# Performance work log

Measured on AMD Instinct MI355X. Metric: run time of the kernel, lower is better.

The kernel has to match this reference:

```python
import jax, jax.numpy as jnp
import numpy as np


def setup_inputs() -> dict:
    key = jax.random.key(0)
    k1, k2, k3 = jax.random.split(key, 3)
    B, C, N, T = 32, 64, 1024, 64
    x = jax.random.normal(k1, (B, C, N, T), dtype=jnp.float32)
    W = jax.random.normal(k2, (T, T), dtype=jnp.float32) * 0.05
    alpha = jax.random.normal(k3, (C,), dtype=jnp.float32) * 0.1
    return {"x": x, "W": W, "alpha": alpha}


def reference(x, W, alpha):
    # x: [B, C, N, T]; channel-weighted reduction -> Q = K: [B, N, T]
    q = jnp.einsum('bcnt,c->bnt', x, alpha)
    # bilinear scores: K @ W @ Q^T -> [B, N, N]
    scores = jnp.einsum('bnt,ts,bms->bnm', q, W, q)
    return jax.nn.softmax(scores, axis=-1)
```

## Files before the change

### kernel.cpp

```cpp
#include <hip/hip_runtime.h>

#define B_ 32
#define C_ 64
#define N_ 1024
#define T_ 64

typedef __attribute__((ext_vector_type(8))) _Float16 half8;
typedef __attribute__((ext_vector_type(4))) _Float16 half4;
typedef __attribute__((ext_vector_type(4))) float f32x4;

__global__ __launch_bounds__(256) void k_q(const float* __restrict__ x,
                                           const float* __restrict__ alpha,
                                           _Float16* __restrict__ q_h) {
    const int bid = blockIdx.x;
    const int s1  = (bid & 7) * 256 + (bid >> 3);
    const int b   = s1 >> 6;
    const int n0  = (s1 & 63) * 16;
    const int tid = threadIdx.x;

    const f32x4* xb = (const f32x4*)(x + (size_t)b * C_ * N_ * T_
                                       + (size_t)n0 * T_);
    f32x4 acc = {0.f, 0.f, 0.f, 0.f};
#pragma unroll 4
    for (int c = 0; c < C_; ++c) {
        f32x4 v = __builtin_nontemporal_load(&xb[(size_t)c * (N_ * T_ / 4) + tid]);
        const float ac = alpha[c];
        acc[0] += ac * v[0]; acc[1] += ac * v[1];
        acc[2] += ac * v[2]; acc[3] += ac * v[3];
    }

    half4 h;
#pragma unroll
    for (int j = 0; j < 4; ++j) h[j] = (_Float16)acc[j];
    *(half4*)(q_h + ((size_t)b * N_ + n0) * T_ + (size_t)tid * 4) = h;
}

__global__ __launch_bounds__(512, 4) void k_scores_softmax(
        const _Float16* __restrict__ q_h,
        const float* __restrict__ W,
        float* __restrict__ out) {
    const int bid = blockIdx.x;
    const int s   = (bid & 7) * 64 + (bid >> 3);
    const int b   = s >> 4;
    const int n0  = (s & 15) * 64;
    const int tid  = threadIdx.x;
    const int w    = tid >> 6;
    const int lane = tid & 63;
    const int lr   = lane & 15;
    const int lk   = lane >> 4;

    __shared__ float Ws[T_][T_];
    __shared__ _Float16 qwh[64][72];
    __shared__ float red[2][16][8];

    {
        const f32x4* Wv = (const f32x4*)W;
        f32x4* Wd = (f32x4*)&Ws[0][0];
        Wd[tid]       = Wv[tid];
        Wd[tid + 512] = Wv[tid + 512];
    }
    __syncthreads();

    {
        const int tc  = w & 3;
        const int tr0 = (w >> 2) * 2;
        half8 bh0, bh1, bl0, bl1;
#pragma unroll
        for (int j = 0; j < 8; ++j) {
            const float wv0 = Ws[lk * 8 + j][tc * 16 + lr];
            const float wv1 = Ws[lk * 8 + 32 + j][tc * 16 + lr];
            const _Float16 h0 = (_Float16)wv0;
            const _Float16 h1 = (_Float16)wv1;
            bh0[j] = h0; bl0[j] = (_Float16)(wv0 - (float)h0);
            bh1[j] = h1; bl1[j] = (_Float16)(wv1 - (float)h1);
        }
#pragma unroll
        for (int i = 0; i < 2; ++i) {
            const int tr = tr0 + i;
            const size_t ar = ((size_t)b * N_ + n0 + tr * 16 + lr) * T_ + lk * 8;
            half8 a0 = *(const half8*)(q_h + ar);
            half8 a1 = *(const half8*)(q_h + ar + 32);
            f32x4 a = {0.f, 0.f, 0.f, 0.f};
            a = __builtin_amdgcn_mfma_f32_16x16x32_f16(a0, bh0, a, 0, 0, 0);
            a = __builtin_amdgcn_mfma_f32_16x16x32_f16(a1, bh1, a, 0, 0, 0);
            a = __builtin_amdgcn_mfma_f32_16x16x32_f16(a0, bl0, a, 0, 0, 0);
            a = __builtin_amdgcn_mfma_f32_16x16x32_f16(a1, bl1, a, 0, 0, 0);
#pragma unroll
            for (int r = 0; r < 4; ++r)
                qwh[tr * 16 + lk * 4 + r][tc * 16 + lr] = (_Float16)a[r];
        }
    }

    half8 bst0[8], bst1[8];
    {
        const size_t cb0 = ((size_t)b * N_ + w * 128 + lr) * T_ + lk * 8;
#pragma unroll
        for (int cf = 0; cf < 8; ++cf) {
            bst0[cf] = *(const half8*)(q_h + cb0 + (size_t)cf * 16 * T_);
            bst1[cf] = *(const half8*)(q_h + cb0 + (size_t)cf * 16 * T_ + 32);
        }
    }
    __syncthreads();

    float* const obase = out + ((size_t)b * N_ + n0 + lr) * N_ + w * 128 + lk * 4;

#pragma unroll 1
    for (int g = 0; g < 4; ++g) {
        half8 af0 = *(const half8*)&qwh[g * 16 + lr][lk * 8];
        half8 af1 = *(const half8*)&qwh[g * 16 + lr][lk * 8 + 32];

        f32x4 acc[8];
#pragma unroll
        for (int cf = 0; cf < 8; ++cf) {
            f32x4 a = {0.f, 0.f, 0.f, 0.f};
            a = __builtin_amdgcn_mfma_f32_16x16x32_f16(bst0[cf], af0, a, 0, 0, 0);
            a = __builtin_amdgcn_mfma_f32_16x16x32_f16(bst1[cf], af1, a, 0, 0, 0);
            acc[cf] = a;
        }

        float ssum = 0.f;
#pragma unroll
        for (int cf = 0; cf < 8; ++cf) {
#pragma unroll
            for (int r = 0; r < 4; ++r) {
                float e = __expf(acc[cf][r]);
                acc[cf][r] = e;
                ssum += e;
            }
        }
        ssum += __shfl_xor(ssum, 16);
        ssum += __shfl_xor(ssum, 32);
        if (lane < 16) red[g & 1][lr][w] = ssum;

        asm volatile("s_waitcnt lgkmcnt(0)" ::: "memory");
        __builtin_amdgcn_s_barrier();
        asm volatile("" ::: "memory");

        f32x4 p0 = *(f32x4*)&red[g & 1][lr][0];
        f32x4 p1 = *(f32x4*)&red[g & 1][lr][4];
        const float inv = 1.0f / (p0[0] + p0[1] + p0[2] + p0[3] +
                                  p1[0] + p1[1] + p1[2] + p1[3]);
        f32x4* orow = (f32x4*)(obase + (size_t)g * 16 * N_);
#pragma unroll
        for (int cf = 0; cf < 8; ++cf) {
            f32x4 v = acc[cf];
            v[0] *= inv; v[1] *= inv; v[2] *= inv; v[3] *= inv;
            orow[cf * 4] = v;
        }
    }
}

extern "C" void kernel_launch(void* const* d_in, const int* in_sizes, int n_in,
                              void* d_out, int out_size, void* d_ws, size_t ws_size,
                              hipStream_t stream) {
    const float* x     = (const float*)d_in[0];
    const float* W     = (const float*)d_in[1];
    const float* alpha = (const float*)d_in[2];
    float* out = (float*)d_out;

    _Float16* q_h = (_Float16*)d_ws;

    k_q<<<2048, 256, 0, stream>>>(x, alpha, q_h);
    k_scores_softmax<<<512, 512, 0, stream>>>(q_h, W, out);
}
```

Before: 116.9 us.

## Move q·W projection into reduction kernel and stash result in output buffer

The q·W product (a split-f16 MFMA over W) moves from the scores kernel into the channel-reduction kernel, where each block already holds its 16 q rows. The projected rows are written as f16 into the first bytes of each output row and read back by the scores kernel, which no longer loads W or does the prologue MFMAs. In exchange, every k_q block now loads all of W into shared memory and adds a barrier. The scratch is overwritten by the final softmax stores of the same rows, so it depends on each block reading its rows before writing them.

```diff
diff --git a/kernel.cpp b/kernel.cpp
--- a/kernel.cpp
+++ b/kernel.cpp
@@ -10,13 +10,27 @@
 typedef __attribute__((ext_vector_type(4))) float f32x4;
 
 __global__ __launch_bounds__(256) void k_q(const float* __restrict__ x,
+                                           const float* __restrict__ W,
                                            const float* __restrict__ alpha,
-                                           _Float16* __restrict__ q_h) {
+                                           _Float16* __restrict__ q_h,
+                                           float* __restrict__ out) {
     const int bid = blockIdx.x;
     const int s1  = (bid & 7) * 256 + (bid >> 3);
     const int b   = s1 >> 6;
     const int n0  = (s1 & 63) * 16;
     const int tid = threadIdx.x;
+
+    __shared__ float Ws[T_][T_];
+    __shared__ _Float16 qsh[16][72];
+
+    {
+        const f32x4* Wv = (const f32x4*)W;
+        f32x4* Wd = (f32x4*)&Ws[0][0];
+        Wd[tid]       = Wv[tid];
+        Wd[tid + 256] = Wv[tid + 256];
+        Wd[tid + 512] = Wv[tid + 512];
+        Wd[tid + 768] = Wv[tid + 768];
+    }
 
     const f32x4* xb = (const f32x4*)(x + (size_t)b * C_ * N_ * T_
                                        + (size_t)n0 * T_);
@@ -33,11 +47,44 @@
 #pragma unroll
     for (int j = 0; j < 4; ++j) h[j] = (_Float16)acc[j];
     *(half4*)(q_h + ((size_t)b * N_ + n0) * T_ + (size_t)tid * 4) = h;
+
+    *(half4*)&qsh[tid >> 4][(tid & 15) * 4] = h;
+    __syncthreads();
+
+    {
+        const int w    = tid >> 6;
+        const int lane = tid & 63;
+        const int lr   = lane & 15;
+        const int lk   = lane >> 4;
+
+        half8 a0 = *(const half8*)&qsh[lr][lk * 8];
+        half8 a1 = *(const half8*)&qsh[lr][lk * 8 + 32];
+        half8 bh0, bh1, bl0, bl1;
+#pragma unroll
+        for (int j = 0; j < 8; ++j) {
+            const float wv0 = Ws[lk * 8 + j][w * 16 + lr];
+            const float wv1 = Ws[lk * 8 + 32 + j][w * 16 + lr];
+            const _Float16 h0 = (_Float16)wv0;
+            const _Float16 h1 = (_Float16)wv1;
+            bh0[j] = h0; bl0[j] = (_Float16)(wv0 - (float)h0);
+            bh1[j] = h1; bl1[j] = (_Float16)(wv1 - (float)h1);
+        }
+        f32x4 a = {0.f, 0.f, 0.f, 0.f};
+        a = __builtin_amdgcn_mfma_f32_16x16x32_f16(a0, bh0, a, 0, 0, 0);
+        a = __builtin_amdgcn_mfma_f32_16x16x32_f16(a1, bh1, a, 0, 0, 0);
+        a = __builtin_amdgcn_mfma_f32_16x16x32_f16(a0, bl0, a, 0, 0, 0);
+        a = __builtin_amdgcn_mfma_f32_16x16x32_f16(a1, bl1, a, 0, 0, 0);
+
+        char* sb = (char*)out
+                 + ((size_t)(b * N_ + n0 + lk * 4) * N_) * 4 + (w * 16 + lr) * 2;
+#pragma unroll
+        for (int r = 0; r < 4; ++r)
+            *(_Float16*)(sb + (size_t)r * N_ * 4) = (_Float16)a[r];
+    }
 }
 
 __global__ __launch_bounds__(512, 4) void k_scores_softmax(
         const _Float16* __restrict__ q_h,
-        const float* __restrict__ W,
         float* __restrict__ out) {
     const int bid = blockIdx.x;
     const int s   = (bid & 7) * 64 + (bid >> 3);
@@ -49,46 +96,15 @@
     const int lr   = lane & 15;
     const int lk   = lane >> 4;
 
-    __shared__ float Ws[T_][T_];
     __shared__ _Float16 qwh[64][72];
     __shared__ float red[2][16][8];
 
     {
-        const f32x4* Wv = (const f32x4*)W;
-        f32x4* Wd = (f32x4*)&Ws[0][0];
-        Wd[tid]       = Wv[tid];
-        Wd[tid + 512] = Wv[tid + 512];
-    }
-    __syncthreads();
-
-    {
-        const int tc  = w & 3;
-        const int tr0 = (w >> 2) * 2;
-        half8 bh0, bh1, bl0, bl1;
-#pragma unroll
-        for (int j = 0; j < 8; ++j) {
-            const float wv0 = Ws[lk * 8 + j][tc * 16 + lr];
-            const float wv1 = Ws[lk * 8 + 32 + j][tc * 16 + lr];
-            const _Float16 h0 = (_Float16)wv0;
-            const _Float16 h1 = (_Float16)wv1;
-            bh0[j] = h0; bl0[j] = (_Float16)(wv0 - (float)h0);
-            bh1[j] = h1; bl1[j] = (_Float16)(wv1 - (float)h1);
-        }
-#pragma unroll
-        for (int i = 0; i < 2; ++i) {
-            const int tr = tr0 + i;
-            const size_t ar = ((size_t)b * N_ + n0 + tr * 16 + lr) * T_ + lk * 8;
-            half8 a0 = *(const half8*)(q_h + ar);
-            half8 a1 = *(const half8*)(q_h + ar + 32);
-            f32x4 a = {0.f, 0.f, 0.f, 0.f};
-            a = __builtin_amdgcn_mfma_f32_16x16x32_f16(a0, bh0, a, 0, 0, 0);
-            a = __builtin_amdgcn_mfma_f32_16x16x32_f16(a1, bh1, a, 0, 0, 0);
-            a = __builtin_amdgcn_mfma_f32_16x16x32_f16(a0, bl0, a, 0, 0, 0);
-            a = __builtin_amdgcn_mfma_f32_16x16x32_f16(a1, bl1, a, 0, 0, 0);
-#pragma unroll
-            for (int r = 0; r < 4; ++r)
-                qwh[tr * 16 + lk * 4 + r][tc * 16 + lr] = (_Float16)a[r];
-        }
+        const int r  = tid >> 3;
+        const int c8 = (tid & 7) * 8;
+        half8 hv = *(const half8*)((const char*)out
+                     + ((size_t)(b * N_ + n0 + r) * N_) * 4 + (size_t)c8 * 2);
+        *(half8*)&qwh[r][c8] = hv;
     }
 
     half8 bst0[8], bst1[8];
@@ -160,6 +176,6 @@
 
     _Float16* q_h = (_Float16*)d_ws;
 
-    k_q<<<2048, 256, 0, stream>>>(x, alpha, q_h);
-    k_scores_softmax<<<512, 512, 0, stream>>>(q_h, W, out);
+    k_q<<<2048, 256, 0, stream>>>(x, W, alpha, q_h, out);
+    k_scores_softmax<<<512, 512, 0, stream>>>(q_h, out);
 }
```

Result: no change. 118.2 us (+1.1%).

## Fuse channel reduction into scores kernel with per-batch atomic flag sync

Applied to the files above, without the earlier changes.

Merges the channel-weighted reduction kernel into the scores/softmax kernel. Each block computes its 64 rows of q, writes them to global memory and to shared memory, then waits on a per-batch atomic counter until all 16 blocks of that batch have published their rows before loading the full q. This removes a kernel launch boundary and the global re-read of the block's own q rows, and lets the x read overlap with other blocks' score work. The cost is a spin-wait that relies on all 16 blocks of a batch being co-resident, which risks deadlock or stalls, plus an extra tiny init kernel.

```diff
diff --git a/kernel.cpp b/kernel.cpp
--- a/kernel.cpp
+++ b/kernel.cpp
@@ -9,36 +9,18 @@
 typedef __attribute__((ext_vector_type(4))) _Float16 half4;
 typedef __attribute__((ext_vector_type(4))) float f32x4;
 
-__global__ __launch_bounds__(256) void k_q(const float* __restrict__ x,
-                                           const float* __restrict__ alpha,
-                                           _Float16* __restrict__ q_h) {
-    const int bid = blockIdx.x;
-    const int s1  = (bid & 7) * 256 + (bid >> 3);
-    const int b   = s1 >> 6;
-    const int n0  = (s1 & 63) * 16;
-    const int tid = threadIdx.x;
 
-    const f32x4* xb = (const f32x4*)(x + (size_t)b * C_ * N_ * T_
-                                       + (size_t)n0 * T_);
-    f32x4 acc = {0.f, 0.f, 0.f, 0.f};
-#pragma unroll 4
-    for (int c = 0; c < C_; ++c) {
-        f32x4 v = __builtin_nontemporal_load(&xb[(size_t)c * (N_ * T_ / 4) + tid]);
-        const float ac = alpha[c];
-        acc[0] += ac * v[0]; acc[1] += ac * v[1];
-        acc[2] += ac * v[2]; acc[3] += ac * v[3];
-    }
-
-    half4 h;
-#pragma unroll
-    for (int j = 0; j < 4; ++j) h[j] = (_Float16)acc[j];
-    *(half4*)(q_h + ((size_t)b * N_ + n0) * T_ + (size_t)tid * 4) = h;
+__global__ void k_init(int* flags) {
+    if (threadIdx.x < 32) flags[threadIdx.x] = 0;
 }
 
-__global__ __launch_bounds__(512, 4) void k_scores_softmax(
-        const _Float16* __restrict__ q_h,
+__global__ __launch_bounds__(512, 4) void k_fused(
+        const float* __restrict__ x,
         const float* __restrict__ W,
-        float* __restrict__ out) {
+        const float* __restrict__ alpha,
+        float* __restrict__ out,
+        _Float16* __restrict__ q_h,
+        int* __restrict__ flags) {
     const int bid = blockIdx.x;
     const int s   = (bid & 7) * 64 + (bid >> 3);
     const int b   = s >> 4;
@@ -50,6 +32,7 @@
     const int lk   = lane >> 4;
 
     __shared__ float Ws[T_][T_];
+    __shared__ _Float16 qsh[64][72];
     __shared__ _Float16 qwh[64][72];
     __shared__ float red[2][16][8];
 
@@ -58,6 +41,34 @@
         f32x4* Wd = (f32x4*)&Ws[0][0];
         Wd[tid]       = Wv[tid];
         Wd[tid + 512] = Wv[tid + 512];
+    }
+
+    {
+        const f32x4* xb = (const f32x4*)(x + (size_t)b * C_ * N_ * T_
+                                           + (size_t)n0 * T_);
+        f32x4 acc0 = {0.f, 0.f, 0.f, 0.f};
+        f32x4 acc1 = {0.f, 0.f, 0.f, 0.f};
+#pragma unroll 4
+        for (int c = 0; c < C_; ++c) {
+            const f32x4* xc = xb + (size_t)c * (N_ * T_ / 4);
+            f32x4 v0 = __builtin_nontemporal_load(xc + tid);
+            f32x4 v1 = __builtin_nontemporal_load(xc + tid + 512);
+            const float ac = alpha[c];
+            acc0[0] += ac * v0[0]; acc0[1] += ac * v0[1];
+            acc0[2] += ac * v0[2]; acc0[3] += ac * v0[3];
+            acc1[0] += ac * v1[0]; acc1[1] += ac * v1[1];
+            acc1[2] += ac * v1[2]; acc1[3] += ac * v1[3];
+        }
+        const int r0 = tid >> 4;
+        const int c4 = (tid & 15) * 4;
+        half4 h0, h1;
+#pragma unroll
+        for (int j = 0; j < 4; ++j) { h0[j] = (_Float16)acc0[j];
+                                      h1[j] = (_Float16)acc1[j]; }
+        *(half4*)(q_h + ((size_t)b * N_ + n0 + r0) * T_ + c4)      = h0;
+        *(half4*)(q_h + ((size_t)b * N_ + n0 + r0 + 32) * T_ + c4) = h1;
+        *(half4*)&qsh[r0][c4]      = h0;
+        *(half4*)&qsh[r0 + 32][c4] = h1;
     }
     __syncthreads();
 
@@ -77,9 +88,8 @@
 #pragma unroll
         for (int i = 0; i < 2; ++i) {
             const int tr = tr0 + i;
-            const size_t ar = ((size_t)b * N_ + n0 + tr * 16 + lr) * T_ + lk * 8;
-            half8 a0 = *(const half8*)(q_h + ar);
-            half8 a1 = *(const half8*)(q_h + ar + 32);
+            half8 a0 = *(const half8*)&qsh[tr * 16 + lr][lk * 8];
+            half8 a1 = *(const half8*)&qsh[tr * 16 + lr][lk * 8 + 32];
             f32x4 a = {0.f, 0.f, 0.f, 0.f};
             a = __builtin_amdgcn_mfma_f32_16x16x32_f16(a0, bh0, a, 0, 0, 0);
             a = __builtin_amdgcn_mfma_f32_16x16x32_f16(a1, bh1, a, 0, 0, 0);
@@ -91,6 +101,17 @@
         }
     }
 
+    if (tid == 0) {
+        __threadfence();
+        __hip_atomic_fetch_add(&flags[b], 1,
+                               __ATOMIC_RELEASE, __HIP_MEMORY_SCOPE_AGENT);
+        while (__hip_atomic_load(&flags[b], __ATOMIC_RELAXED,
+                                 __HIP_MEMORY_SCOPE_AGENT) < 16)
+            __builtin_amdgcn_s_sleep(2);
+        __threadfence();
+    }
+    __syncthreads();
+
     half8 bst0[8], bst1[8];
     {
         const size_t cb0 = ((size_t)b * N_ + w * 128 + lr) * T_ + lk * 8;
@@ -100,7 +121,6 @@
             bst1[cf] = *(const half8*)(q_h + cb0 + (size_t)cf * 16 * T_ + 32);
         }
     }
-    __syncthreads();
 
     float* const obase = out + ((size_t)b * N_ + n0 + lr) * N_ + w * 128 + lk * 4;
 
@@ -159,7 +179,8 @@
     float* out = (float*)d_out;
 
     _Float16* q_h = (_Float16*)d_ws;
+    int* flags    = (int*)((char*)d_ws + (4u << 20));
 
-    k_q<<<2048, 256, 0, stream>>>(x, alpha, q_h);
-    k_scores_softmax<<<512, 512, 0, stream>>>(q_h, W, out);
+    k_init<<<1, 32, 0, stream>>>(flags);
+    k_fused<<<512, 512, 0, stream>>>(x, W, alpha, out, q_h, flags);
 }
```

After: 192.5 us. 1.65x slower.
